# Performance work log

Measured on AMD Instinct MI355X. Metric: run time of the kernel, lower is better.

Reference implementation:

```python
import jax, jax.numpy as jnp
import numpy as np
import math

B, S, DM = 32, 512, 1024   # batch (= groups*channels), seq_len, d_model
H, D, C = 16, 64, 8        # n_heads, d_kv, n_channels
NB, MD = 32, 128           # relative_attention_num_buckets, max_distance


def setup_inputs() -> dict:
    key = jax.random.key(0)
    ks = jax.random.split(key, 7)
    return {
        "hidden_states": jax.random.normal(ks[0], (B, S, DM), jnp.float32),
        "Wq": jax.random.normal(ks[1], (DM, H * D), jnp.float32) * 0.02,
        "Wk": jax.random.normal(ks[2], (DM, H * D), jnp.float32) * 0.02,
        "Wv": jax.random.normal(ks[3], (DM, H * D), jnp.float32) * 0.02,
        "Wo": jax.random.normal(ks[4], (H * D, DM), jnp.float32) * 0.02,
        "rel_emb": jax.random.normal(ks[5], (NB, H), jnp.float32) * 0.02,
        "beta": jax.random.normal(ks[6], (1, 1, H, 1, 1), jnp.float32) * 0.01,
    }


def _rel_bucket(relative_position, num_buckets=NB, max_distance=MD):
    # bidirectional (encoder) bucketing, faithful to T5
    nb = num_buckets // 2
    buckets = (relative_position > 0).astype(jnp.int32) * nb
    rp = jnp.abs(relative_position)
    max_exact = nb // 2
    is_small = rp < max_exact
    rp_safe = jnp.maximum(rp, 1).astype(jnp.float32)
    large = max_exact + (
        jnp.log(rp_safe / max_exact) / math.log(max_distance / max_exact) * (nb - max_exact)
    ).astype(jnp.int32)
    large = jnp.minimum(large, nb - 1)
    return buckets + jnp.where(is_small, rp, large)


def reference(hidden_states, Wq, Wk, Wv, Wo, rel_emb, beta):
    G = B // C  # groups

    def proj(W):
        # (B,S,DM) -> (B,S,H,D) -> (B,H,S,D) -> (G,C,H,S,D)
        x = (hidden_states @ W).reshape(B, S, H, D).transpose(0, 2, 1, 3)
        return x.reshape(G, C, H, S, D)

    q, k, v = proj(Wq), proj(Wk), proj(Wv)

    # relative position bias: (1,1,H,S,S)
    rel_pos = jnp.arange(S)[None, :] - jnp.arange(S)[:, None]
    bias = rel_emb[_rel_bucket(rel_pos)].transpose(2, 0, 1)[None, None]

    # local (dot-product) attention, T5-style: no 1/sqrt(d) scaling
    scores = jnp.einsum('gchsd,gchtd->gchst', q, k) + bias
    attn_w = jax.nn.softmax(scores, axis=-1)
    a_dot = jnp.einsum('gchst,gchtd->gchsd', attn_w, v)

    # compressive memory: ELU+1 feature map, summed over channels
    sk = jax.nn.elu(k) + 1.0
    M = jnp.einsum('gchsd,gchse->ghde', sk, v)   # (G,H,D,D)
    z = sk.sum(axis=3).sum(axis=1)               # (G,H,D)
    sq = jax.nn.elu(q) + 1.0
    num = jnp.einsum('gchsd,ghde->gchse', sq, M)
    den = jnp.einsum('gchsd,ghd->gchs', sq, z)[..., None] + 1e-6
    a_mem = num / den

    gate = jax.nn.sigmoid(beta)  # (1,1,H,1,1)
    out = gate * a_mem + (1.0 - gate) * a_dot

    # (G,C,H,S,D) -> (B,H,S,D) -> (B,S,H*D)
    out = out.reshape(B, H, S, D).transpose(0, 2, 1, 3).reshape(B, S, H * D)
    return out @ Wo
```

## Files before the change

### kernel.cpp

```cpp
#include <hip/hip_runtime.h>
#include <stdint.h>

typedef unsigned short u16;
typedef u16 u16x8 __attribute__((ext_vector_type(8)));
typedef u16 u16x4 __attribute__((ext_vector_type(4)));
typedef __bf16 bf16x8 __attribute__((ext_vector_type(8)));
typedef float f32x4 __attribute__((ext_vector_type(4)));

#define DEV static __device__ __forceinline__

DEV u16 f2bf(float f) {
  union { float f; uint32_t u; } v; v.f = f;
  uint32_t r = v.u + 0x7FFFu + ((v.u >> 16) & 1u);
  return (u16)(r >> 16);
}
DEV float bf2f(u16 s) {
  union { uint32_t u; float f; } v; v.u = ((uint32_t)s) << 16;
  return v.f;
}
DEV float elu1(float x) { return x > 0.f ? x + 1.f : __expf(x); }
DEV u16x8 ld8u(const u16* p) { return *reinterpret_cast<const u16x8*>(p); }

DEV f32x4 mfma16(u16x8 a, u16x8 b, f32x4 c) {
  return __builtin_amdgcn_mfma_f32_16x16x32_bf16(
      __builtin_bit_cast(bf16x8, a), __builtin_bit_cast(bf16x8, b), c, 0, 0, 0);
}
DEV void async16(void* lds, const void* g) {
  __builtin_amdgcn_global_load_lds(
      (__attribute__((address_space(1))) void*)g,
      (__attribute__((address_space(3))) void*)lds, 16, 0, 0);
}

#define BARR __builtin_amdgcn_s_barrier()
#define LG0  asm volatile("s_waitcnt lgkmcnt(0)" ::: "memory")
#define VMC(N) asm volatile("s_waitcnt vmcnt(" #N ")" ::: "memory")


__global__ __launch_bounds__(256) void k_cvt(const float* __restrict__ in, u16* __restrict__ out) {
  int i = blockIdx.x * 256 + threadIdx.x;
  const float4* p = reinterpret_cast<const float4*>(in) + (size_t)i * 2;
  float4 a = p[0], b = p[1];
  u16x8 o;
  o[0] = f2bf(a.x); o[1] = f2bf(a.y); o[2] = f2bf(a.z); o[3] = f2bf(a.w);
  o[4] = f2bf(b.x); o[5] = f2bf(b.y); o[6] = f2bf(b.z); o[7] = f2bf(b.w);
  reinterpret_cast<u16x8*>(out)[i] = o;
}

__global__ __launch_bounds__(1024) void k_tr(const float* __restrict__ Wq, const float* __restrict__ Wk,
                                             const float* __restrict__ Wv, const float* __restrict__ Wo,
                                             u16* __restrict__ wt, u16* __restrict__ wot) {
  __shared__ float tb[32][33];
  int mat = blockIdx.x >> 10;
  int tile = blockIdx.x & 1023;
  int n0 = (tile >> 5) * 32;
  int k0 = (tile & 31) * 32;
  const float* W = (mat == 0) ? Wq : (mat == 1) ? Wk : (mat == 2) ? Wv : Wo;
  int tx = threadIdx.x & 31, ty = threadIdx.x >> 5;
  tb[ty][tx] = W[(size_t)(k0 + ty) * 1024 + n0 + tx];
  __syncthreads();
  u16 v = f2bf(tb[tx][ty]);
  if (mat < 3) wt[(size_t)(mat * 1024 + n0 + ty) * 1024 + k0 + tx] = v;
  else         wot[(size_t)(n0 + ty) * 1024 + k0 + tx] = v;
}

__global__ void k_bias(const float* __restrict__ rel, float* __restrict__ bias) {
  int off = blockIdx.x * 256 + threadIdx.x;
  if (off >= 1023) return;
  int rp = off - 511;
  int bck = rp > 0 ? 16 : 0;
  int arp = rp < 0 ? -rp : rp;
  int idx;
  if (arp < 8) idx = arp;
  else {
    float l = logf((float)arp * 0.125f) / logf(16.0f) * 8.0f;
    int lg = 8 + (int)l;
    idx = lg < 15 ? lg : 15;
  }
  bck += idx;
  for (int h = 0; h < 16; ++h) bias[h * 1023 + off] = rel[bck * 16 + h];
}


template <int EPI, int NSQN>
__global__ __launch_bounds__(512, 2) void k_g256(const u16* __restrict__ A, const u16* __restrict__ Bt,
                                                 u16* __restrict__ oq, u16* __restrict__ ok2,
                                                 u16* __restrict__ ovt, float* __restrict__ of) {
  __shared__ __align__(16) u16 lsA[2][256 * 64];
  __shared__ __align__(16) u16 lsB[2][256 * 64];
  const int t = threadIdx.x;
  const int lane = t & 63, w = t >> 6;
  const int wm = w >> 2, wn = w & 3;
  const int lr = lane & 15, lg = lane >> 4;

  const int bid = blockIdx.x;
  const int xcd = bid & 7, local = bid >> 3;
  const int s = local >> 4, w16 = local & 15;
  const int m0 = (xcd * 8 + (s / NSQN) * 4 + (w16 >> 2)) * 256;
  const int n0 = ((s % NSQN) * 4 + (w16 & 3)) * 256;

  auto stage = [&](int kt, int slot) {
    const int k0 = kt * 64;
#pragma unroll
    for (int i = 0; i < 4; ++i) {
      int c = i * 512 + t;
      int row = c >> 3, u = c & 7;
      int us = (u ^ (row & 7)) << 3;
      async16(&lsA[slot][c * 8], A + (size_t)(m0 + row) * 1024 + k0 + us);
      async16(&lsB[slot][c * 8], Bt + (size_t)(n0 + row) * 1024 + k0 + us);
    }
  };

  f32x4 acc[8][4];
#pragma unroll
  for (int i = 0; i < 8; ++i)
#pragma unroll
    for (int j = 0; j < 4; ++j) acc[i][j] = (f32x4){0.f, 0.f, 0.f, 0.f};

  stage(0, 0);
  stage(1, 1);
  VMC(8);
  BARR;

  for (int kt = 0; kt < 16; ++kt) {
    const int slot = kt & 1;
    const u16* la = &lsA[slot][0];
    const u16* lb = &lsB[slot][0];

    u16x8 bf[4][2], af[4][2];
#pragma unroll
    for (int ni = 0; ni < 4; ++ni) {
      const int r = wn * 64 + ni * 16 + lr;
#pragma unroll
      for (int kk = 0; kk < 2; ++kk)
        bf[ni][kk] = ld8u(lb + r * 64 + (((kk * 4 + lg) ^ (r & 7)) << 3));
    }
#pragma unroll
    for (int mi = 0; mi < 4; ++mi) {
      const int r = wm * 128 + mi * 16 + lr;
#pragma unroll
      for (int kk = 0; kk < 2; ++kk)
        af[mi][kk] = ld8u(la + r * 64 + (((kk * 4 + lg) ^ (r & 7)) << 3));
    }
    __builtin_amdgcn_s_setprio(1);
#pragma unroll
    for (int mi = 0; mi < 4; ++mi)
#pragma unroll
      for (int ni = 0; ni < 4; ++ni)
#pragma unroll
        for (int kk = 0; kk < 2; ++kk)
          acc[mi][ni] = mfma16(af[mi][kk], bf[ni][kk], acc[mi][ni]);
    __builtin_amdgcn_s_setprio(0);

    u16x8 af2[4][2];
#pragma unroll
    for (int mi = 0; mi < 4; ++mi) {
      const int r = wm * 128 + 64 + mi * 16 + lr;
#pragma unroll
      for (int kk = 0; kk < 2; ++kk)
        af2[mi][kk] = ld8u(la + r * 64 + (((kk * 4 + lg) ^ (r & 7)) << 3));
    }
    LG0;
    BARR;
    if (kt + 2 < 16) stage(kt + 2, slot);

    __builtin_amdgcn_s_setprio(1);
#pragma unroll
    for (int mi = 0; mi < 4; ++mi)
#pragma unroll
      for (int ni = 0; ni < 4; ++ni)
#pragma unroll
        for (int kk = 0; kk < 2; ++kk)
          acc[4 + mi][ni] = mfma16(af2[mi][kk], bf[ni][kk], acc[4 + mi][ni]);
    __builtin_amdgcn_s_setprio(0);

    if (kt + 2 < 16) { VMC(8); }
    else             { VMC(0); }
    BARR;
  }

  if (EPI == 0) {
    const int which = n0 >> 10;
    const int nb = (n0 & 1023) + wn * 64;
#pragma unroll
    for (int mi = 0; mi < 8; ++mi)
#pragma unroll
      for (int r = 0; r < 4; ++r) {
        int m = m0 + wm * 128 + mi * 16 + lg * 4 + r;
        int b = m >> 9, s2 = m & 511;
#pragma unroll
        for (int ni = 0; ni < 4; ++ni) {
          int nc = nb + ni * 16 + lr;
          int h = nc >> 6, d = nc & 63;
          int bh = b * 16 + h;
          u16 v = f2bf(acc[mi][ni][r]);
          if (which == 0)      oq[(size_t)(bh * 512 + s2) * 64 + d] = v;
          else if (which == 1) ok2[(size_t)(bh * 512 + s2) * 64 + d] = v;
          else                 ovt[(size_t)(bh * 64 + d) * 512 + s2] = v;
        }
      }
  } else {
#pragma unroll
    for (int mi = 0; mi < 8; ++mi)
#pragma unroll
      for (int r = 0; r < 4; ++r) {
        int m = m0 + wm * 128 + mi * 16 + lg * 4 + r;
#pragma unroll
        for (int ni = 0; ni < 4; ++ni) {
          int n = n0 + wn * 64 + ni * 16 + lr;
          of[(size_t)m * 1024 + n] = acc[mi][ni][r];
        }
      }
  }
}


__global__ __launch_bounds__(256) void k_mem(const u16* __restrict__ K, const u16* __restrict__ Vt,
                                             float* __restrict__ Mp, float* __restrict__ zp) {
  __shared__ __align__(16) u16 skT[64 * 128];
  __shared__ __align__(16) u16 lV[64 * 128];
  __shared__ float mbuf[64][65];
  __shared__ float zsh[4][64];
  const int bid = blockIdx.x;
  const int g = bid >> 7, h = (bid >> 3) & 15, c = bid & 7;
  const int bh = (g * 8 + c) * 16 + h;
  const u16* kp = K + (size_t)bh * 512 * 64;
  const u16* vp = Vt + (size_t)bh * 64 * 512;
  const int t = threadIdx.x, lane = t & 63, w = t >> 6;
  const int lr = lane & 15, lg = lane >> 4;
  const int dmy = t & 63, sq = t >> 6;

  f32x4 acc[4][4];
#pragma unroll
  for (int i = 0; i < 4; ++i)
#pragma unroll
    for (int j = 0; j < 4; ++j) acc[i][j] = (f32x4){0.f, 0.f, 0.f, 0.f};
  float zacc = 0.f;

  for (int s0 = 0; s0 < 512; s0 += 128) {
#pragma unroll
    for (int i = 0; i < 4; ++i) {
      int c2 = i * 256 + t;
      int row = c2 >> 4, u = c2 & 15;
      async16(lV + c2 * 8, vp + (size_t)row * 512 + s0 + ((u ^ (row & 7)) << 3));
    }
#pragma unroll
    for (int r = 0; r < 4; ++r) {
      const int un = sq + r * 4;
      const int ss0 = un * 8;
      u16x8 vals;
#pragma unroll
      for (int j = 0; j < 8; ++j) {
        float x = elu1(bf2f(kp[(size_t)(s0 + ss0 + j) * 64 + dmy]));
        zacc += x;
        vals[j] = f2bf(x);
      }
      *reinterpret_cast<u16x8*>(skT + dmy * 128 + ((un ^ (dmy & 7)) << 3)) = vals;
    }
    VMC(0);
    __syncthreads();
    u16x8 af[4], bfv[4];
#pragma unroll
    for (int ds = 0; ds < 4; ++ds) {
      const int d = ds * 16 + lr;
      af[ds] = ld8u(skT + d * 128 + (((w * 4 + lg) ^ (d & 7)) << 3));
    }
#pragma unroll
    for (int es = 0; es < 4; ++es) {
      const int e = es * 16 + lr;
      bfv[es] = ld8u(lV + e * 128 + (((w * 4 + lg) ^ (e & 7)) << 3));
    }
#pragma unroll
    for (int ds = 0; ds < 4; ++ds)
#pragma unroll
      for (int es = 0; es < 4; ++es) acc[ds][es] = mfma16(af[ds], bfv[es], acc[ds][es]);
    __syncthreads();
  }

  zsh[sq][dmy] = zacc;
  for (int wv = 0; wv < 4; ++wv) {
    if (w == wv) {
#pragma unroll
      for (int ds = 0; ds < 4; ++ds)
#pragma unroll
        for (int es = 0; es < 4; ++es)
#pragma unroll
          for (int r = 0; r < 4; ++r) {
            int d = ds * 16 + lg * 4 + r, e = es * 16 + lr;
            if (wv == 0) mbuf[d][e] = acc[ds][es][r];
            else         mbuf[d][e] += acc[ds][es][r];
          }
    }
    __syncthreads();
  }
#pragma unroll
  for (int j = 0; j < 16; ++j) {
    int idx = j * 256 + t;
    Mp[(size_t)bid * 4096 + idx] = mbuf[idx >> 6][idx & 63];
  }
  if (t < 64) zp[(size_t)bid * 64 + t] = zsh[0][t] + zsh[1][t] + zsh[2][t] + zsh[3][t];
}

__global__ __launch_bounds__(256) void k_red(const float* __restrict__ Mp, const float* __restrict__ zp,
                                             u16* __restrict__ Mt, float* __restrict__ zv) {
  const int gh = blockIdx.x;
  const int t = threadIdx.x;
#pragma unroll
  for (int j = 0; j < 16; ++j) {
    int idx = j * 256 + t;
    int d = idx >> 6, e = idx & 63;
    float s = 0.f;
#pragma unroll
    for (int c = 0; c < 8; ++c) s += Mp[(size_t)(gh * 8 + c) * 4096 + idx];
    Mt[(size_t)gh * 4096 + e * 64 + d] = f2bf(s);
  }
  if (t < 64) {
    float s = 0.f;
#pragma unroll
    for (int c = 0; c < 8; ++c) s += zp[(size_t)(gh * 8 + c) * 64 + t];
    zv[gh * 64 + t] = s;
  }
}


__global__ __launch_bounds__(256, 4) void k_attn(const u16* __restrict__ Q, const u16* __restrict__ K,
                                                 const u16* __restrict__ Vt, const u16* __restrict__ Mt,
                                                 const float* __restrict__ zv, const float* __restrict__ bias,
                                                 const float* __restrict__ beta, u16* __restrict__ blend) {
  __shared__ __align__(16) u16 lK[64 * 64];
  __shared__ __align__(16) u16 lV[64 * 64];
  __shared__ __align__(16) u16 ps[4][32 * 64];
  __shared__ float lbias[1023];
  __shared__ float zs[64];
  __shared__ float rsl[4][32];
  __shared__ float dnl[4][32];

  const int bid = blockIdx.x;
  const int bh = bid >> 2, qg = bid & 3;
  const int b = bh >> 4, h = bh & 15, g = b >> 3;
  const int gh = g * 16 + h;
  const int t = threadIdx.x, lane = t & 63, w = t >> 6;
  const int lr = lane & 15, lg = lane >> 4;
  const int q0w = qg * 128 + w * 32;
  const u16* qp = Q + (size_t)bh * 512 * 64;
  const u16* kp = K + (size_t)bh * 512 * 64;
  const u16* vp = Vt + (size_t)bh * 64 * 512;
  const u16* mp = Mt + (size_t)gh * 4096;
  const float gate = 1.f / (1.f + __expf(-beta[h]));
  u16* psw = &ps[w][0];

  for (int i = t; i < 1023; i += 256) lbias[i] = bias[h * 1023 + i];
  if (t < 64) zs[t] = zv[gh * 64 + t];

  u16x8 qf[2][2];
#pragma unroll
  for (int qs = 0; qs < 2; ++qs)
#pragma unroll
    for (int dc = 0; dc < 2; ++dc)
      qf[qs][dc] = ld8u(qp + (size_t)(q0w + qs * 16 + lr) * 64 + dc * 32 + lg * 8);

#pragma unroll
  for (int i = 0; i < 2; ++i) {
    int c = w * 128 + i * 64 + lane;
    int kr = c >> 3, u = c & 7;
    async16(lK + c * 8, kp + (size_t)kr * 64 + ((u ^ (kr & 7)) << 3));
    async16(lV + c * 8, vp + (size_t)kr * 512 + ((u ^ (kr & 7)) << 3));
  }
  __syncthreads();

#pragma unroll
  for (int qs = 0; qs < 2; ++qs) {
    float sum = 0.f;
#pragma unroll
    for (int dc = 0; dc < 2; ++dc)
#pragma unroll
      for (int j = 0; j < 8; ++j)
        sum += elu1(bf2f(qf[qs][dc][j])) * zs[dc * 32 + lg * 8 + j];
    sum += __shfl_xor(sum, 16, 64);
    sum += __shfl_xor(sum, 32, 64);
    if (lane < 16) dnl[w][qs * 16 + lane] = sum + 1e-6f;
  }

  f32x4 acc[2][4];
#pragma unroll
  for (int qs = 0; qs < 2; ++qs)
#pragma unroll
    for (int es = 0; es < 4; ++es) acc[qs][es] = (f32x4){0.f, 0.f, 0.f, 0.f};
  float rs[2] = {0.f, 0.f};

  for (int kt = 0; kt < 8; ++kt) {
#pragma unroll
    for (int ks = 0; ks < 4; ++ks) {
      const int kr = ks * 16 + lr;
      u16x8 kf0 = ld8u(lK + kr * 64 + (((0 * 4 + lg) ^ (kr & 7)) << 3));
      u16x8 kf1 = ld8u(lK + kr * 64 + (((1 * 4 + lg) ^ (kr & 7)) << 3));
#pragma unroll
      for (int qs = 0; qs < 2; ++qs) {
        f32x4 s = mfma16(kf0, qf[qs][0], (f32x4){0.f, 0.f, 0.f, 0.f});
        s = mfma16(kf1, qf[qs][1], s);
        const int bbase = kt * 64 + ks * 16 + lg * 4 - (q0w + qs * 16 + lr) + 511;
        u16x4 pk;
        float lsum = 0.f;
#pragma unroll
        for (int r = 0; r < 4; ++r) {
          float p = __expf(s[r] + lbias[bbase + r]);
          lsum += p;
          pk[r] = f2bf(p);
        }
        rs[qs] += lsum;
        const int row = qs * 16 + lr;
        const int addr = row * 64 + (((ks * 2 + (lg >> 1)) ^ (row & 7)) << 3) + (lg & 1) * 4;
        *reinterpret_cast<u16x4*>(psw + addr) = pk;
      }
    }
#pragma unroll
    for (int kc = 0; kc < 2; ++kc) {
      u16x8 pf[2];
#pragma unroll
      for (int qs = 0; qs < 2; ++qs) {
        const int row = qs * 16 + lr;
        pf[qs] = ld8u(psw + row * 64 + (((kc * 4 + lg) ^ (row & 7)) << 3));
      }
#pragma unroll
      for (int es = 0; es < 4; ++es) {
        const int er = es * 16 + lr;
        u16x8 vf = ld8u(lV + er * 64 + (((kc * 4 + lg) ^ (er & 7)) << 3));
#pragma unroll
        for (int qs = 0; qs < 2; ++qs) acc[qs][es] = mfma16(pf[qs], vf, acc[qs][es]);
      }
    }
    __syncthreads();
    if (kt + 1 < 8) {
#pragma unroll
      for (int i = 0; i < 2; ++i) {
        int c = w * 128 + i * 64 + lane;
        int kr = c >> 3, u = c & 7;
        async16(lK + c * 8, kp + (size_t)((kt + 1) * 64 + kr) * 64 + ((u ^ (kr & 7)) << 3));
        async16(lV + c * 8, vp + (size_t)kr * 512 + (kt + 1) * 64 + ((u ^ (kr & 7)) << 3));
      }
    }
    __syncthreads();
  }

#pragma unroll
  for (int qs = 0; qs < 2; ++qs) {
    float v = rs[qs];
    v += __shfl_xor(v, 16, 64);
    v += __shfl_xor(v, 32, 64);
    if (lane < 16) rsl[w][qs * 16 + lane] = 1.f / v;
  }

  u16x8 sqf[2][2];
#pragma unroll
  for (int qs = 0; qs < 2; ++qs)
#pragma unroll
    for (int dc = 0; dc < 2; ++dc)
#pragma unroll
      for (int j = 0; j < 8; ++j) sqf[qs][dc][j] = f2bf(elu1(bf2f(qf[qs][dc][j])));
  f32x4 am[2][4];
#pragma unroll
  for (int qs = 0; qs < 2; ++qs)
#pragma unroll
    for (int es = 0; es < 4; ++es) am[qs][es] = (f32x4){0.f, 0.f, 0.f, 0.f};
#pragma unroll
  for (int es = 0; es < 4; ++es)
#pragma unroll
    for (int dc = 0; dc < 2; ++dc) {
      u16x8 mf = ld8u(mp + (es * 16 + lr) * 64 + dc * 32 + lg * 8);
#pragma unroll
      for (int qs = 0; qs < 2; ++qs) am[qs][es] = mfma16(sqf[qs][dc], mf, am[qs][es]);
    }

#pragma unroll
  for (int qs = 0; qs < 2; ++qs)
#pragma unroll
    for (int r = 0; r < 4; ++r) {
      const int rowl = qs * 16 + lg * 4 + r;
      const float rinv = rsl[w][rowl];
      const float den = dnl[w][rowl];
      const int q = q0w + rowl;
#pragma unroll
      for (int es = 0; es < 4; ++es) {
        float o = gate * (am[qs][es][r] / den) + (1.f - gate) * acc[qs][es][r] * rinv;
        blend[(size_t)(b * 512 + q) * 1024 + h * 64 + es * 16 + lr] = f2bf(o);
      }
    }
}


extern "C" void kernel_launch(void* const* d_in, const int* in_sizes, int n_in,
                              void* d_out, int out_size, void* d_ws, size_t ws_size,
                              hipStream_t stream) {
  (void)in_sizes; (void)n_in; (void)out_size; (void)ws_size;
  const float* hs   = (const float*)d_in[0];
  const float* Wq   = (const float*)d_in[1];
  const float* Wk   = (const float*)d_in[2];
  const float* Wv   = (const float*)d_in[3];
  const float* Wo   = (const float*)d_in[4];
  const float* rel  = (const float*)d_in[5];
  const float* beta = (const float*)d_in[6];
  float* out = (float*)d_out;

  char* ws = (char*)d_ws;
  size_t off = 0;
  auto alloc = [&](size_t bytes) -> char* {
    char* p = ws + off;
    off += (bytes + 255) & ~(size_t)255;
    return p;
  };
  u16* hsb    = (u16*)alloc(16384ull * 1024 * 2);
  u16* wt     = (u16*)alloc(3072ull * 1024 * 2);
  u16* wot    = (u16*)alloc(1024ull * 1024 * 2);
  u16* q      = (u16*)alloc(16384ull * 1024 * 2);
  u16* k      = (u16*)alloc(16384ull * 1024 * 2);
  u16* vt     = (u16*)alloc(16384ull * 1024 * 2);
  float* Mp   = (float*)alloc(512ull * 4096 * 4);
  float* zp   = (float*)alloc(512ull * 64 * 4);
  u16* Mt     = (u16*)alloc(64ull * 4096 * 2);
  float* zv   = (float*)alloc(64ull * 64 * 4);
  float* bias = (float*)alloc(16ull * 1023 * 4);
  u16* blend  = hsb;

  k_cvt<<<8192, 256, 0, stream>>>(hs, hsb);
  k_tr<<<4096, 1024, 0, stream>>>(Wq, Wk, Wv, Wo, wt, wot);
  k_bias<<<4, 256, 0, stream>>>(rel, bias);
  k_g256<0, 3><<<768, 512, 0, stream>>>(hsb, wt, q, k, vt, nullptr);
  k_mem<<<512, 256, 0, stream>>>(k, vt, Mp, zp);
  k_red<<<64, 256, 0, stream>>>(Mp, zp, Mt, zv);
  k_attn<<<2048, 256, 0, stream>>>(q, k, vt, Mt, zv, bias, beta, blend);
  k_g256<1, 1><<<256, 512, 0, stream>>>(blend, wot, nullptr, nullptr, nullptr, out);
}
```

Measured before the change: 356.5 us.

## Shrink GEMM tiles to 128x256 with K-step 32 for higher occupancy

Reworks the bf16 MFMA GEMM used for the QKV and output projections. The block tile goes from 256x256 with K=64 to 128x256 with K=32, using a new LDS swizzle that packs two rows per 64-element line. This cuts LDS use and registers so three blocks fit per CU, and doubles the grid (1536 and 512 blocks), aiming for better wave-level parallelism and tail balance on the smaller output GEMM. In exchange, per-block operand reuse drops and there are twice as many barrier-synchronised K iterations.

```diff
diff --git a/kernel.cpp b/kernel.cpp
--- a/kernel.cpp
+++ b/kernel.cpp
@@ -81,12 +81,12 @@
 }
 
 
-template <int EPI, int NSQN>
-__global__ __launch_bounds__(512, 2) void k_g256(const u16* __restrict__ A, const u16* __restrict__ Bt,
+template <int EPI>
+__global__ __launch_bounds__(512, 3) void k_g256(const u16* __restrict__ A, const u16* __restrict__ Bt,
                                                  u16* __restrict__ oq, u16* __restrict__ ok2,
                                                  u16* __restrict__ ovt, float* __restrict__ of) {
-  __shared__ __align__(16) u16 lsA[2][256 * 64];
-  __shared__ __align__(16) u16 lsB[2][256 * 64];
+  __shared__ __align__(16) u16 lsA[2][128 * 32];
+  __shared__ __align__(16) u16 lsB[2][256 * 32];
   const int t = threadIdx.x;
   const int lane = t & 63, w = t >> 6;
   const int wm = w >> 2, wn = w & 3;
@@ -95,86 +95,63 @@
   const int bid = blockIdx.x;
   const int xcd = bid & 7, local = bid >> 3;
   const int s = local >> 4, w16 = local & 15;
-  const int m0 = (xcd * 8 + (s / NSQN) * 4 + (w16 >> 2)) * 256;
-  const int n0 = ((s % NSQN) * 4 + (w16 & 3)) * 256;
+  const int msq = s & 3, nsq = s >> 2;
+  const int m0 = (xcd * 16 + msq * 4 + (w16 >> 2)) * 128;
+  const int n0 = (nsq * 4 + (w16 & 3)) * 256;
 
   auto stage = [&](int kt, int slot) {
-    const int k0 = kt * 64;
-#pragma unroll
-    for (int i = 0; i < 4; ++i) {
-      int c = i * 512 + t;
-      int row = c >> 3, u = c & 7;
-      int us = (u ^ (row & 7)) << 3;
-      async16(&lsA[slot][c * 8], A + (size_t)(m0 + row) * 1024 + k0 + us);
-      async16(&lsB[slot][c * 8], Bt + (size_t)(n0 + row) * 1024 + k0 + us);
+    const int k0 = kt * 32;
+    {
+      int c = t, S = c >> 3, q = (c & 7) ^ (S & 7);
+      int row = 2 * S + (q >> 2), u = q & 3;
+      async16(&lsA[slot][c * 8], A + (size_t)(m0 + row) * 1024 + k0 + u * 8);
+    }
+#pragma unroll
+    for (int i = 0; i < 2; ++i) {
+      int c = i * 512 + t, S = c >> 3, q = (c & 7) ^ (S & 7);
+      int row = 2 * S + (q >> 2), u = q & 3;
+      async16(&lsB[slot][c * 8], Bt + (size_t)(n0 + row) * 1024 + k0 + u * 8);
     }
   };
-
-  f32x4 acc[8][4];
-#pragma unroll
-  for (int i = 0; i < 8; ++i)
+  auto rdoff = [&](int r_) -> int {
+    return (r_ >> 1) * 64 + (((((r_ & 1) << 2) + lg) ^ ((r_ >> 1) & 7)) << 3);
+  };
+
+  f32x4 acc[4][4];
+#pragma unroll
+  for (int i = 0; i < 4; ++i)
 #pragma unroll
     for (int j = 0; j < 4; ++j) acc[i][j] = (f32x4){0.f, 0.f, 0.f, 0.f};
 
   stage(0, 0);
   stage(1, 1);
-  VMC(8);
+  VMC(3);
   BARR;
 
-  for (int kt = 0; kt < 16; ++kt) {
+  for (int kt = 0; kt < 32; ++kt) {
     const int slot = kt & 1;
     const u16* la = &lsA[slot][0];
     const u16* lb = &lsB[slot][0];
 
-    u16x8 bf[4][2], af[4][2];
-#pragma unroll
-    for (int ni = 0; ni < 4; ++ni) {
-      const int r = wn * 64 + ni * 16 + lr;
-#pragma unroll
-      for (int kk = 0; kk < 2; ++kk)
-        bf[ni][kk] = ld8u(lb + r * 64 + (((kk * 4 + lg) ^ (r & 7)) << 3));
-    }
-#pragma unroll
-    for (int mi = 0; mi < 4; ++mi) {
-      const int r = wm * 128 + mi * 16 + lr;
-#pragma unroll
-      for (int kk = 0; kk < 2; ++kk)
-        af[mi][kk] = ld8u(la + r * 64 + (((kk * 4 + lg) ^ (r & 7)) << 3));
-    }
-    __builtin_amdgcn_s_setprio(1);
-#pragma unroll
-    for (int mi = 0; mi < 4; ++mi)
-#pragma unroll
-      for (int ni = 0; ni < 4; ++ni)
-#pragma unroll
-        for (int kk = 0; kk < 2; ++kk)
-          acc[mi][ni] = mfma16(af[mi][kk], bf[ni][kk], acc[mi][ni]);
-    __builtin_amdgcn_s_setprio(0);
-
-    u16x8 af2[4][2];
-#pragma unroll
-    for (int mi = 0; mi < 4; ++mi) {
-      const int r = wm * 128 + 64 + mi * 16 + lr;
-#pragma unroll
-      for (int kk = 0; kk < 2; ++kk)
-        af2[mi][kk] = ld8u(la + r * 64 + (((kk * 4 + lg) ^ (r & 7)) << 3));
-    }
+    u16x8 af[4], bf[4];
+#pragma unroll
+    for (int mi = 0; mi < 4; ++mi) af[mi] = ld8u(la + rdoff(wm * 64 + mi * 16 + lr));
+#pragma unroll
+    for (int ni = 0; ni < 4; ++ni) bf[ni] = ld8u(lb + rdoff(wn * 64 + ni * 16 + lr));
     LG0;
     BARR;
-    if (kt + 2 < 16) stage(kt + 2, slot);
+    if (kt + 2 < 32) stage(kt + 2, slot);
 
     __builtin_amdgcn_s_setprio(1);
 #pragma unroll
     for (int mi = 0; mi < 4; ++mi)
 #pragma unroll
       for (int ni = 0; ni < 4; ++ni)
-#pragma unroll
-        for (int kk = 0; kk < 2; ++kk)
-          acc[4 + mi][ni] = mfma16(af2[mi][kk], bf[ni][kk], acc[4 + mi][ni]);
+        acc[mi][ni] = mfma16(af[mi], bf[ni], acc[mi][ni]);
     __builtin_amdgcn_s_setprio(0);
 
-    if (kt + 2 < 16) { VMC(8); }
-    else             { VMC(0); }
+    if (kt + 2 < 32)      { VMC(3); }
+    else if (kt == 30)    { VMC(0); }
     BARR;
   }
 
@@ -182,10 +159,10 @@
     const int which = n0 >> 10;
     const int nb = (n0 & 1023) + wn * 64;
 #pragma unroll
-    for (int mi = 0; mi < 8; ++mi)
+    for (int mi = 0; mi < 4; ++mi)
 #pragma unroll
       for (int r = 0; r < 4; ++r) {
-        int m = m0 + wm * 128 + mi * 16 + lg * 4 + r;
+        int m = m0 + wm * 64 + mi * 16 + lg * 4 + r;
         int b = m >> 9, s2 = m & 511;
 #pragma unroll
         for (int ni = 0; ni < 4; ++ni) {
@@ -200,10 +177,10 @@
       }
   } else {
 #pragma unroll
-    for (int mi = 0; mi < 8; ++mi)
+    for (int mi = 0; mi < 4; ++mi)
 #pragma unroll
       for (int r = 0; r < 4; ++r) {
-        int m = m0 + wm * 128 + mi * 16 + lg * 4 + r;
+        int m = m0 + wm * 64 + mi * 16 + lg * 4 + r;
 #pragma unroll
         for (int ni = 0; ni < 4; ++ni) {
           int n = n0 + wn * 64 + ni * 16 + lr;
@@ -523,9 +500,9 @@
   k_cvt<<<8192, 256, 0, stream>>>(hs, hsb);
   k_tr<<<4096, 1024, 0, stream>>>(Wq, Wk, Wv, Wo, wt, wot);
   k_bias<<<4, 256, 0, stream>>>(rel, bias);
-  k_g256<0, 3><<<768, 512, 0, stream>>>(hsb, wt, q, k, vt, nullptr);
+  k_g256<0><<<1536, 512, 0, stream>>>(hsb, wt, q, k, vt, nullptr);
   k_mem<<<512, 256, 0, stream>>>(k, vt, Mp, zp);
   k_red<<<64, 256, 0, stream>>>(Mp, zp, Mt, zv);
   k_attn<<<2048, 256, 0, stream>>>(q, k, vt, Mt, zv, bias, beta, blend);
-  k_g256<1, 1><<<256, 512, 0, stream>>>(blend, wot, nullptr, nullptr, nullptr, out);
-}
+  k_g256<1><<<512, 512, 0, stream>>>(blend, wot, nullptr, nullptr, nullptr, out);
+}
```

After: 341.7 us. 4.1% less time.
